# Kernel tuning notes

Hardware: AMD Instinct MI355X
Metric: run time of the kernel (lower is better)

Reference implementation:

```python
import jax, jax.numpy as jnp
import numpy as np

WS = 8          # window size
NUM_HEADS = 8


def setup_inputs() -> dict:
    key = jax.random.key(0)
    k1, k2, k3 = jax.random.split(key, 3)
    B, H, W, C = 8, 192, 192, 256
    x = jax.random.normal(k1, (B, H, W, C), dtype=jnp.float32)
    w_qkv = jax.random.normal(k2, (3 * C, C), dtype=jnp.float32) * (C ** -0.5)
    b_qkv = jnp.zeros((3 * C,), dtype=jnp.float32)
    w_proj = jax.random.normal(k3, (C, C), dtype=jnp.float32) * (C ** -0.5)
    b_proj = jnp.zeros((C,), dtype=jnp.float32)
    return {"x": x, "w_qkv": w_qkv, "b_qkv": b_qkv, "w_proj": w_proj, "b_proj": b_proj}


def _mhsa(tokens, w_qkv, b_qkv, w_proj, b_proj):
    # tokens: [Bgrp, N, C]
    Bg, N, C = tokens.shape
    d = C // NUM_HEADS
    qkv = tokens @ w_qkv.T + b_qkv                      # [Bg, N, 3C]
    qkv = qkv.reshape(Bg, N, 3, NUM_HEADS, d)
    q, k, v = [jnp.transpose(qkv[:, :, i], (0, 2, 1, 3)) for i in range(3)]  # [Bg, h, N, d]
    attn = jax.nn.softmax(jnp.einsum('bhnd,bhmd->bhnm', q, k) * (d ** -0.5), axis=-1)
    out = jnp.einsum('bhnm,bhmd->bhnd', attn, v)        # [Bg, h, N, d]
    out = jnp.transpose(out, (0, 2, 1, 3)).reshape(Bg, N, C)
    return out @ w_proj.T + b_proj


def reference(x, w_qkv, b_qkv, w_proj, b_proj):
    B, H, W, C = x.shape
    nH, nW = H // WS, W // WS
    # window partition: [B, H, W, C] -> [B*nH*nW, WS, WS, C]
    g = x.reshape(B, nH, WS, nW, WS, C).transpose(0, 1, 3, 2, 4, 5)
    tokens = g.reshape(B * nH * nW, WS * WS, C)
    tokens = _mhsa(tokens, w_qkv, b_qkv, w_proj, b_proj)
    # window unpartition
    g = tokens.reshape(B, nH, nW, WS, WS, C).transpose(0, 1, 3, 2, 4, 5)
    return g.reshape(B, H, W, C)
```

## Files before the change

### kernel.cpp

```cpp
#include <hip/hip_runtime.h>

typedef _Float16 half8  __attribute__((ext_vector_type(8)));
typedef _Float16 half4_t __attribute__((ext_vector_type(4)));
typedef __fp16   fp16x2 __attribute__((ext_vector_type(2)));
typedef float    f32x4  __attribute__((ext_vector_type(4)));

union PKU  { fp16x2 h; int i; };
union PK2  { fp16x2 h[2]; int i[2]; half4_t h4; };

__device__ __forceinline__ half4_t mk4(int a, int b) {
  PK2 u; u.i[0] = a; u.i[1] = b; return u.h4;
}

__device__ __forceinline__ int tokIdx(int r, int c) { return r*256 + (c ^ ((r & 7) << 3)); }

__global__ void __launch_bounds__(256)
wconv_kernel(const float* __restrict__ wq, const float* __restrict__ wp,
             _Float16* __restrict__ o)
{
  const int i = (blockIdx.x * 256 + threadIdx.x) * 8;
  const float4 a = *(const float4*)((i < 768*256 ? wq + i : wp + (i - 768*256)));
  const float4 b = *(const float4*)((i < 768*256 ? wq + i + 4 : wp + (i - 768*256) + 4));
  half8 h;
  h[0] = (_Float16)a.x; h[1] = (_Float16)a.y; h[2] = (_Float16)a.z; h[3] = (_Float16)a.w;
  h[4] = (_Float16)b.x; h[5] = (_Float16)b.y; h[6] = (_Float16)b.z; h[7] = (_Float16)b.w;
  *(half8*)(o + i) = h;
}

__global__ void __launch_bounds__(256, 3)
attn_kernel(const float* __restrict__ x,
            const float* __restrict__ b_qkv,
            const float* __restrict__ b_proj,
            const _Float16* __restrict__ w16,
            float* __restrict__ out)
{
  __shared__ __align__(16) _Float16 tok[64*256];

  const int tid  = threadIdx.x;
  const int lane = tid & 63;
  const int w    = tid >> 6;
  const int l15  = lane & 15;
  const int g    = lane >> 4;

  const int wid = blockIdx.x;
  const int b   = wid / (24*24);
  const int wh  = (wid / 24) % 24;
  const int ww  = wid % 24;
  const long long base = (((long long)b*192 + wh*8)*192 + ww*8)*256;

#pragma unroll
  for (int i = 0; i < 16; ++i) {
    const int tk = w*16 + i;
    const f32x4 v = *(const f32x4*)(x + base + ((tk >> 3)*192 + (tk & 7))*256 + lane*4);
    half4_t h;
    h[0] = (_Float16)v[0]; h[1] = (_Float16)v[1];
    h[2] = (_Float16)v[2]; h[3] = (_Float16)v[3];
    *(half4_t*)(tok + tk*256 + ((lane*4) ^ ((tk & 7) << 3))) = h;
  }
  __syncthreads();

  const _Float16* wqkv16  = w16;
  const _Float16* wproj16 = w16 + 768*256;

  const float ALPHA = 0.17677669529663687f;

  int ohp[2][2][4][2];

#pragma unroll
  for (int hi = 0; hi < 2; ++hi) {
    const int hd = 2*w + hi;

    int qtp[2][4][2], kcp[2][4][2];
    {
      f32x4 qa[2][4], kc[2][4];
#pragma unroll
      for (int mi = 0; mi < 2; ++mi) {
        const f32x4 bqv = *(const f32x4*)(b_qkv + hd*32 + mi*16 + g*4);
        const f32x4 bkv = *(const f32x4*)(b_qkv + 256 + hd*32 + mi*16 + g*4);
#pragma unroll
        for (int ni = 0; ni < 4; ++ni) { qa[mi][ni] = bqv; kc[mi][ni] = bkv; }
      }
#pragma unroll
      for (int kk = 0; kk < 8; ++kk) {
        half8 bt[4], awq[2], awk[2];
#pragma unroll
        for (int ni = 0; ni < 4; ++ni)
          bt[ni] = *(const half8*)(tok + tokIdx(ni*16 + l15, kk*32 + g*8));
#pragma unroll
        for (int mi = 0; mi < 2; ++mi) {
          awq[mi] = *(const half8*)(wqkv16 + (      hd*32 + mi*16 + l15)*256 + kk*32 + g*8);
          awk[mi] = *(const half8*)(wqkv16 + (256 + hd*32 + mi*16 + l15)*256 + kk*32 + g*8);
        }
        __builtin_amdgcn_s_setprio(1);
#pragma unroll
        for (int mi = 0; mi < 2; ++mi)
#pragma unroll
          for (int ni = 0; ni < 4; ++ni) {
            qa[mi][ni] = __builtin_amdgcn_mfma_f32_16x16x32_f16(awq[mi], bt[ni], qa[mi][ni], 0, 0, 0);
            kc[mi][ni] = __builtin_amdgcn_mfma_f32_16x16x32_f16(awk[mi], bt[ni], kc[mi][ni], 0, 0, 0);
          }
        __builtin_amdgcn_s_setprio(0);
      }
#pragma unroll
      for (int mi = 0; mi < 2; ++mi)
#pragma unroll
        for (int ni = 0; ni < 4; ++ni) {
          PKU q0, q1, k0, k1;
          q0.h = __builtin_amdgcn_cvt_pkrtz(qa[mi][ni][0]*ALPHA, qa[mi][ni][1]*ALPHA);
          q1.h = __builtin_amdgcn_cvt_pkrtz(qa[mi][ni][2]*ALPHA, qa[mi][ni][3]*ALPHA);
          k0.h = __builtin_amdgcn_cvt_pkrtz(kc[mi][ni][0], kc[mi][ni][1]);
          k1.h = __builtin_amdgcn_cvt_pkrtz(kc[mi][ni][2], kc[mi][ni][3]);
          qtp[mi][ni][0] = q0.i; qtp[mi][ni][1] = q1.i;
          kcp[mi][ni][0] = k0.i; kcp[mi][ni][1] = k1.i;
        }
    }

    int pk[4][4][2];
    float rv[4];
#pragma unroll
    for (int pr = 0; pr < 2; ++pr) {
      f32x4 s[4][2];
#pragma unroll
      for (int MI = 0; MI < 4; ++MI)
#pragma unroll
        for (int nj = 0; nj < 2; ++nj) s[MI][nj] = (f32x4)0.0f;
      __builtin_amdgcn_s_setprio(1);
#pragma unroll
      for (int kk2 = 0; kk2 < 2; ++kk2)
#pragma unroll
        for (int nj = 0; nj < 2; ++nj) {
          const int ni = pr*2 + nj;
          const half4_t qb = mk4(qtp[kk2][ni][0], qtp[kk2][ni][1]);
#pragma unroll
          for (int MI = 0; MI < 4; ++MI)
            s[MI][nj] = __builtin_amdgcn_mfma_f32_16x16x16f16(
                mk4(kcp[kk2][MI][0], kcp[kk2][MI][1]), qb, s[MI][nj], 0, 0, 0);
        }
      __builtin_amdgcn_s_setprio(0);

#pragma unroll
      for (int nj = 0; nj < 2; ++nj) {
        const int ni = pr*2 + nj;
        float mm[4];
#pragma unroll
        for (int MI = 0; MI < 4; ++MI)
          mm[MI] = fmaxf(fmaxf(s[MI][nj][0], s[MI][nj][1]), fmaxf(s[MI][nj][2], s[MI][nj][3]));
        float m = fmaxf(fmaxf(mm[0], mm[1]), fmaxf(mm[2], mm[3]));
        m = fmaxf(m, __shfl_xor(m, 16, 64));
        m = fmaxf(m, __shfl_xor(m, 32, 64));
        float ss[4];
#pragma unroll
        for (int MI = 0; MI < 4; ++MI) {
#pragma unroll
          for (int r = 0; r < 4; ++r) s[MI][nj][r] = __expf(s[MI][nj][r] - m);
          ss[MI] = (s[MI][nj][0] + s[MI][nj][1]) + (s[MI][nj][2] + s[MI][nj][3]);
        }
        float sum = (ss[0] + ss[1]) + (ss[2] + ss[3]);
        sum += __shfl_xor(sum, 16, 64);
        sum += __shfl_xor(sum, 32, 64);
        rv[ni] = 1.0f / sum;
#pragma unroll
        for (int MI = 0; MI < 4; ++MI) {
          PKU u0, u1;
          u0.h = __builtin_amdgcn_cvt_pkrtz(s[MI][nj][0], s[MI][nj][1]);
          u1.h = __builtin_amdgcn_cvt_pkrtz(s[MI][nj][2], s[MI][nj][3]);
          pk[MI][ni][0] = u0.i;
          pk[MI][ni][1] = u1.i;
        }
      }
    }

    int vpk[4][2][2];
    {
      f32x4 vv[4][2];
#pragma unroll
      for (int ni = 0; ni < 2; ++ni) {
        const float bv = b_qkv[512 + hd*32 + ni*16 + l15];
#pragma unroll
        for (int mi = 0; mi < 4; ++mi) vv[mi][ni] = (f32x4)bv;
      }
#pragma unroll
      for (int kk = 0; kk < 8; ++kk) {
        half8 bt[4], wv[2];
#pragma unroll
        for (int mi = 0; mi < 4; ++mi)
          bt[mi] = *(const half8*)(tok + tokIdx(mi*16 + l15, kk*32 + g*8));
#pragma unroll
        for (int ni = 0; ni < 2; ++ni)
          wv[ni] = *(const half8*)(wqkv16 + (512 + hd*32 + ni*16 + l15)*256 + kk*32 + g*8);
        __builtin_amdgcn_s_setprio(1);
#pragma unroll
        for (int mi = 0; mi < 4; ++mi)
#pragma unroll
          for (int ni = 0; ni < 2; ++ni)
            vv[mi][ni] = __builtin_amdgcn_mfma_f32_16x16x32_f16(bt[mi], wv[ni], vv[mi][ni], 0, 0, 0);
        __builtin_amdgcn_s_setprio(0);
      }
#pragma unroll
      for (int ni = 0; ni < 2; ++ni)
#pragma unroll
        for (int mi = 0; mi < 4; ++mi) {
          PKU u0, u1;
          u0.h = __builtin_amdgcn_cvt_pkrtz(vv[mi][ni][0], vv[mi][ni][1]);
          u1.h = __builtin_amdgcn_cvt_pkrtz(vv[mi][ni][2], vv[mi][ni][3]);
          vpk[mi][ni][0] = u0.i;
          vpk[mi][ni][1] = u1.i;
        }
    }

    {
      f32x4 oh[2][4];
#pragma unroll
      for (int MI = 0; MI < 2; ++MI)
#pragma unroll
        for (int ni = 0; ni < 4; ++ni) oh[MI][ni] = (f32x4)0.0f;
      __builtin_amdgcn_s_setprio(1);
#pragma unroll
      for (int kk2 = 0; kk2 < 4; ++kk2)
#pragma unroll
        for (int ni = 0; ni < 4; ++ni) {
          const half4_t pb = mk4(pk[kk2][ni][0], pk[kk2][ni][1]);
#pragma unroll
          for (int MI = 0; MI < 2; ++MI)
            oh[MI][ni] = __builtin_amdgcn_mfma_f32_16x16x16f16(
                mk4(vpk[kk2][MI][0], vpk[kk2][MI][1]), pb, oh[MI][ni], 0, 0, 0);
        }
      __builtin_amdgcn_s_setprio(0);
#pragma unroll
      for (int MI = 0; MI < 2; ++MI)
#pragma unroll
        for (int ni = 0; ni < 4; ++ni) {
          PK2 u;
          u.h[0] = __builtin_amdgcn_cvt_pkrtz(oh[MI][ni][0] * rv[ni], oh[MI][ni][1] * rv[ni]);
          u.h[1] = __builtin_amdgcn_cvt_pkrtz(oh[MI][ni][2] * rv[ni], oh[MI][ni][3] * rv[ni]);
          ohp[hi][MI][ni][0] = u.i[0];
          ohp[hi][MI][ni][1] = u.i[1];
        }
    }
  }

  __syncthreads();

#pragma unroll
  for (int hi = 0; hi < 2; ++hi) {
    const int hd = 2*w + hi;
#pragma unroll
    for (int MI = 0; MI < 2; ++MI)
#pragma unroll
      for (int ni = 0; ni < 4; ++ni) {
        PK2 u;
        u.i[0] = ohp[hi][MI][ni][0];
        u.i[1] = ohp[hi][MI][ni][1];
        *(half4_t*)(tok + tokIdx(ni*16 + l15, hd*32 + MI*16 + g*4)) = u.h4;
      }
  }
  __syncthreads();

  f32x4 pa[4][4];
#pragma unroll
  for (int ni = 0; ni < 4; ++ni) {
    const float bb = b_proj[w*64 + ni*16 + l15];
#pragma unroll
    for (int mi = 0; mi < 4; ++mi) pa[mi][ni] = (f32x4)bb;
  }

#pragma unroll
  for (int kk = 0; kk < 8; ++kk) {
    half8 af[4], bf[4];
#pragma unroll
    for (int mi = 0; mi < 4; ++mi)
      af[mi] = *(const half8*)(tok + tokIdx(mi*16 + l15, kk*32 + g*8));
#pragma unroll
    for (int ni = 0; ni < 4; ++ni)
      bf[ni] = *(const half8*)(wproj16 + (w*64 + ni*16 + l15)*256 + kk*32 + g*8);
    __builtin_amdgcn_s_setprio(1);
#pragma unroll
    for (int mi = 0; mi < 4; ++mi)
#pragma unroll
      for (int ni = 0; ni < 4; ++ni)
        pa[mi][ni] = __builtin_amdgcn_mfma_f32_16x16x32_f16(af[mi], bf[ni], pa[mi][ni], 0, 0, 0);
    __builtin_amdgcn_s_setprio(0);
  }

  float* tokF = (float*)tok;
#pragma unroll
  for (int p = 0; p < 2; ++p) {
    __syncthreads();
#pragma unroll
    for (int mh = 0; mh < 2; ++mh) {
      const int mi = 2*p + mh;
#pragma unroll
      for (int ni = 0; ni < 4; ++ni)
#pragma unroll
        for (int r = 0; r < 4; ++r) {
          const int tr = mh*16 + g*4 + r;
          tokF[tr*256 + ((w*64 + ni*16 + l15) ^ ((tr & 7) << 2))] = pa[mi][ni][r];
        }
    }
    __syncthreads();
#pragma unroll
    for (int i = 0; i < 8; ++i) {
      const int tr = w*8 + i;
      const int t  = p*32 + tr;
      const long long rowbase = base + ((long long)(t >> 3)*192 + (t & 7))*256;
      const f32x4 v4 = *(const f32x4*)(tokF + tr*256 + ((lane*4) ^ ((tr & 7) << 2)));
      *(f32x4*)(out + rowbase + lane*4) = v4;
    }
  }
}

extern "C" void kernel_launch(void* const* d_in, const int* in_sizes, int n_in,
                              void* d_out, int out_size, void* d_ws, size_t ws_size,
                              hipStream_t stream) {
  const float* x      = (const float*)d_in[0];
  const float* w_qkv  = (const float*)d_in[1];
  const float* b_qkv  = (const float*)d_in[2];
  const float* w_proj = (const float*)d_in[3];
  const float* b_proj = (const float*)d_in[4];
  float* out = (float*)d_out;
  _Float16* w16 = (_Float16*)d_ws;

  wconv_kernel<<<128, 256, 0, stream>>>(w_qkv, w_proj, w16);
  attn_kernel<<<4608, 256, 0, stream>>>(x, b_qkv, b_proj, w16, out);
}
```

Before: 337.1 us.

## Interleave V projection MFMAs with softmax of scores to overlap compute

Computes all four score tiles up front, then interleaves the V-projection MFMA steps with the per-column softmax (exp, reductions, shuffles), so that matrix-core work and VALU/transcendental work can overlap within a wave. The setprio hints around the V MFMAs are dropped. Holding all 16 score accumulators live alongside the V accumulators raises register pressure, which could cause spills or lower occupancy under the 3-blocks launch bound.

```diff
diff --git a/kernel.cpp b/kernel.cpp
--- a/kernel.cpp
+++ b/kernel.cpp
@@ -27,6 +27,54 @@
   *(half8*)(o + i) = h;
 }
 
+#define SOFTMAX_NI(ni)                                                          \
+  {                                                                             \
+    float mm0 = fmaxf(fmaxf(s[0][ni][0], s[0][ni][1]), fmaxf(s[0][ni][2], s[0][ni][3])); \
+    float mm1 = fmaxf(fmaxf(s[1][ni][0], s[1][ni][1]), fmaxf(s[1][ni][2], s[1][ni][3])); \
+    float mm2 = fmaxf(fmaxf(s[2][ni][0], s[2][ni][1]), fmaxf(s[2][ni][2], s[2][ni][3])); \
+    float mm3 = fmaxf(fmaxf(s[3][ni][0], s[3][ni][1]), fmaxf(s[3][ni][2], s[3][ni][3])); \
+    float m = fmaxf(fmaxf(mm0, mm1), fmaxf(mm2, mm3));                          \
+    m = fmaxf(m, __shfl_xor(m, 16, 64));                                        \
+    m = fmaxf(m, __shfl_xor(m, 32, 64));                                        \
+    float ss[4];                                                                \
+    _Pragma("unroll")                                                           \
+    for (int MI = 0; MI < 4; ++MI) {                                            \
+      _Pragma("unroll")                                                         \
+      for (int r = 0; r < 4; ++r) s[MI][ni][r] = __expf(s[MI][ni][r] - m);      \
+      ss[MI] = (s[MI][ni][0] + s[MI][ni][1]) + (s[MI][ni][2] + s[MI][ni][3]);   \
+    }                                                                           \
+    float sum = (ss[0] + ss[1]) + (ss[2] + ss[3]);                              \
+    sum += __shfl_xor(sum, 16, 64);                                             \
+    sum += __shfl_xor(sum, 32, 64);                                             \
+    rv[ni] = 1.0f / sum;                                                        \
+    _Pragma("unroll")                                                           \
+    for (int MI = 0; MI < 4; ++MI) {                                            \
+      PKU u0, u1;                                                               \
+      u0.h = __builtin_amdgcn_cvt_pkrtz(s[MI][ni][0], s[MI][ni][1]);            \
+      u1.h = __builtin_amdgcn_cvt_pkrtz(s[MI][ni][2], s[MI][ni][3]);            \
+      pk[MI][ni][0] = u0.i;                                                     \
+      pk[MI][ni][1] = u1.i;                                                     \
+    }                                                                           \
+  }
+
+#define V_STEP(kk)                                                              \
+  {                                                                             \
+    half8 bt0 = *(const half8*)(tok + tokIdx( 0 + l15, (kk)*32 + g*8));         \
+    half8 bt1 = *(const half8*)(tok + tokIdx(16 + l15, (kk)*32 + g*8));         \
+    half8 bt2 = *(const half8*)(tok + tokIdx(32 + l15, (kk)*32 + g*8));         \
+    half8 bt3 = *(const half8*)(tok + tokIdx(48 + l15, (kk)*32 + g*8));         \
+    half8 wv0 = *(const half8*)(wqkv16 + (512 + hd*32 +      l15)*256 + (kk)*32 + g*8); \
+    half8 wv1 = *(const half8*)(wqkv16 + (512 + hd*32 + 16 + l15)*256 + (kk)*32 + g*8); \
+    vv[0][0] = __builtin_amdgcn_mfma_f32_16x16x32_f16(bt0, wv0, vv[0][0], 0, 0, 0); \
+    vv[0][1] = __builtin_amdgcn_mfma_f32_16x16x32_f16(bt0, wv1, vv[0][1], 0, 0, 0); \
+    vv[1][0] = __builtin_amdgcn_mfma_f32_16x16x32_f16(bt1, wv0, vv[1][0], 0, 0, 0); \
+    vv[1][1] = __builtin_amdgcn_mfma_f32_16x16x32_f16(bt1, wv1, vv[1][1], 0, 0, 0); \
+    vv[2][0] = __builtin_amdgcn_mfma_f32_16x16x32_f16(bt2, wv0, vv[2][0], 0, 0, 0); \
+    vv[2][1] = __builtin_amdgcn_mfma_f32_16x16x32_f16(bt2, wv1, vv[2][1], 0, 0, 0); \
+    vv[3][0] = __builtin_amdgcn_mfma_f32_16x16x32_f16(bt3, wv0, vv[3][0], 0, 0, 0); \
+    vv[3][1] = __builtin_amdgcn_mfma_f32_16x16x32_f16(bt3, wv1, vv[3][1], 0, 0, 0); \
+  }
+
 __global__ void __launch_bounds__(256, 3)
 attn_kernel(const float* __restrict__ x,
             const float* __restrict__ b_qkv,
@@ -117,96 +165,57 @@
 
     int pk[4][4][2];
     float rv[4];
-#pragma unroll
-    for (int pr = 0; pr < 2; ++pr) {
-      f32x4 s[4][2];
+    f32x4 vv[4][2];
+    {
+      f32x4 s[4][4];
 #pragma unroll
       for (int MI = 0; MI < 4; ++MI)
 #pragma unroll
-        for (int nj = 0; nj < 2; ++nj) s[MI][nj] = (f32x4)0.0f;
+        for (int ni = 0; ni < 4; ++ni) s[MI][ni] = (f32x4)0.0f;
       __builtin_amdgcn_s_setprio(1);
 #pragma unroll
       for (int kk2 = 0; kk2 < 2; ++kk2)
 #pragma unroll
-        for (int nj = 0; nj < 2; ++nj) {
-          const int ni = pr*2 + nj;
+        for (int ni = 0; ni < 4; ++ni) {
           const half4_t qb = mk4(qtp[kk2][ni][0], qtp[kk2][ni][1]);
 #pragma unroll
           for (int MI = 0; MI < 4; ++MI)
-            s[MI][nj] = __builtin_amdgcn_mfma_f32_16x16x16f16(
-                mk4(kcp[kk2][MI][0], kcp[kk2][MI][1]), qb, s[MI][nj], 0, 0, 0);
+            s[MI][ni] = __builtin_amdgcn_mfma_f32_16x16x16f16(
+                mk4(kcp[kk2][MI][0], kcp[kk2][MI][1]), qb, s[MI][ni], 0, 0, 0);
         }
       __builtin_amdgcn_s_setprio(0);
 
-#pragma unroll
-      for (int nj = 0; nj < 2; ++nj) {
-        const int ni = pr*2 + nj;
-        float mm[4];
-#pragma unroll
-        for (int MI = 0; MI < 4; ++MI)
-          mm[MI] = fmaxf(fmaxf(s[MI][nj][0], s[MI][nj][1]), fmaxf(s[MI][nj][2], s[MI][nj][3]));
-        float m = fmaxf(fmaxf(mm[0], mm[1]), fmaxf(mm[2], mm[3]));
-        m = fmaxf(m, __shfl_xor(m, 16, 64));
-        m = fmaxf(m, __shfl_xor(m, 32, 64));
-        float ss[4];
-#pragma unroll
-        for (int MI = 0; MI < 4; ++MI) {
-#pragma unroll
-          for (int r = 0; r < 4; ++r) s[MI][nj][r] = __expf(s[MI][nj][r] - m);
-          ss[MI] = (s[MI][nj][0] + s[MI][nj][1]) + (s[MI][nj][2] + s[MI][nj][3]);
-        }
-        float sum = (ss[0] + ss[1]) + (ss[2] + ss[3]);
-        sum += __shfl_xor(sum, 16, 64);
-        sum += __shfl_xor(sum, 32, 64);
-        rv[ni] = 1.0f / sum;
-#pragma unroll
-        for (int MI = 0; MI < 4; ++MI) {
-          PKU u0, u1;
-          u0.h = __builtin_amdgcn_cvt_pkrtz(s[MI][nj][0], s[MI][nj][1]);
-          u1.h = __builtin_amdgcn_cvt_pkrtz(s[MI][nj][2], s[MI][nj][3]);
-          pk[MI][ni][0] = u0.i;
-          pk[MI][ni][1] = u1.i;
-        }
-      }
-    }
-
-    int vpk[4][2][2];
-    {
-      f32x4 vv[4][2];
 #pragma unroll
       for (int ni = 0; ni < 2; ++ni) {
         const float bv = b_qkv[512 + hd*32 + ni*16 + l15];
 #pragma unroll
         for (int mi = 0; mi < 4; ++mi) vv[mi][ni] = (f32x4)bv;
       }
-#pragma unroll
-      for (int kk = 0; kk < 8; ++kk) {
-        half8 bt[4], wv[2];
-#pragma unroll
-        for (int mi = 0; mi < 4; ++mi)
-          bt[mi] = *(const half8*)(tok + tokIdx(mi*16 + l15, kk*32 + g*8));
-#pragma unroll
-        for (int ni = 0; ni < 2; ++ni)
-          wv[ni] = *(const half8*)(wqkv16 + (512 + hd*32 + ni*16 + l15)*256 + kk*32 + g*8);
-        __builtin_amdgcn_s_setprio(1);
-#pragma unroll
-        for (int mi = 0; mi < 4; ++mi)
-#pragma unroll
-          for (int ni = 0; ni < 2; ++ni)
-            vv[mi][ni] = __builtin_amdgcn_mfma_f32_16x16x32_f16(bt[mi], wv[ni], vv[mi][ni], 0, 0, 0);
-        __builtin_amdgcn_s_setprio(0);
-      }
-#pragma unroll
-      for (int ni = 0; ni < 2; ++ni)
-#pragma unroll
-        for (int mi = 0; mi < 4; ++mi) {
-          PKU u0, u1;
-          u0.h = __builtin_amdgcn_cvt_pkrtz(vv[mi][ni][0], vv[mi][ni][1]);
-          u1.h = __builtin_amdgcn_cvt_pkrtz(vv[mi][ni][2], vv[mi][ni][3]);
-          vpk[mi][ni][0] = u0.i;
-          vpk[mi][ni][1] = u1.i;
-        }
-    }
+      V_STEP(0)
+      V_STEP(1)
+      SOFTMAX_NI(0)
+      V_STEP(2)
+      V_STEP(3)
+      SOFTMAX_NI(1)
+      V_STEP(4)
+      V_STEP(5)
+      SOFTMAX_NI(2)
+      V_STEP(6)
+      V_STEP(7)
+      SOFTMAX_NI(3)
+    }
+
+    int vpk[4][2][2];
+#pragma unroll
+    for (int ni = 0; ni < 2; ++ni)
+#pragma unroll
+      for (int mi = 0; mi < 4; ++mi) {
+        PKU u0, u1;
+        u0.h = __builtin_amdgcn_cvt_pkrtz(vv[mi][ni][0], vv[mi][ni][1]);
+        u1.h = __builtin_amdgcn_cvt_pkrtz(vv[mi][ni][2], vv[mi][ni][3]);
+        vpk[mi][ni][0] = u0.i;
+        vpk[mi][ni][1] = u1.i;
+      }
 
     {
       f32x4 oh[2][4];
```

After: 352.2 us. 4.5% more time.

## Assign one head per wave with 512-thread blocks for higher occupancy

Applied to the files above, without the earlier changes.

Doubles the block to 8 waves so each wave handles a single attention head instead of two. The Q and K projections are computed in separate phases, and the output projection splits 32 columns per wave. This cuts per-wave register pressure and raises resident waves per CU, which should hide MFMA and LDS latency better. The tighter launch bounds risk register spilling, and the larger blocks add more barrier participants.

```diff
diff --git a/kernel.cpp b/kernel.cpp
--- a/kernel.cpp
+++ b/kernel.cpp
@@ -27,7 +27,7 @@
   *(half8*)(o + i) = h;
 }
 
-__global__ void __launch_bounds__(256, 3)
+__global__ void __launch_bounds__(512, 4)
 attn_kernel(const float* __restrict__ x,
             const float* __restrict__ b_qkv,
             const float* __restrict__ b_proj,
@@ -49,8 +49,8 @@
   const long long base = (((long long)b*192 + wh*8)*192 + ww*8)*256;
 
 #pragma unroll
-  for (int i = 0; i < 16; ++i) {
-    const int tk = w*16 + i;
+  for (int i = 0; i < 8; ++i) {
+    const int tk = w*8 + i;
     const f32x4 v = *(const f32x4*)(x + base + ((tk >> 3)*192 + (tk & 7))*256 + lane*4);
     half4_t h;
     h[0] = (_Float16)v[0]; h[1] = (_Float16)v[1];
@@ -63,221 +63,241 @@
   const _Float16* wproj16 = w16 + 768*256;
 
   const float ALPHA = 0.17677669529663687f;
-
-  int ohp[2][2][4][2];
-
-#pragma unroll
-  for (int hi = 0; hi < 2; ++hi) {
-    const int hd = 2*w + hi;
-
-    int qtp[2][4][2], kcp[2][4][2];
-    {
-      f32x4 qa[2][4], kc[2][4];
-#pragma unroll
-      for (int mi = 0; mi < 2; ++mi) {
-        const f32x4 bqv = *(const f32x4*)(b_qkv + hd*32 + mi*16 + g*4);
-        const f32x4 bkv = *(const f32x4*)(b_qkv + 256 + hd*32 + mi*16 + g*4);
-#pragma unroll
-        for (int ni = 0; ni < 4; ++ni) { qa[mi][ni] = bqv; kc[mi][ni] = bkv; }
-      }
-#pragma unroll
-      for (int kk = 0; kk < 8; ++kk) {
-        half8 bt[4], awq[2], awk[2];
+  const int hd = w;
+
+  int qtp[2][4][2];
+  {
+    f32x4 qa[2][4];
+#pragma unroll
+    for (int mi = 0; mi < 2; ++mi) {
+      const f32x4 bqv = *(const f32x4*)(b_qkv + hd*32 + mi*16 + g*4);
+#pragma unroll
+      for (int ni = 0; ni < 4; ++ni) qa[mi][ni] = bqv;
+    }
+#pragma unroll
+    for (int kk = 0; kk < 8; ++kk) {
+      half8 bt[4], aw[2];
+#pragma unroll
+      for (int ni = 0; ni < 4; ++ni)
+        bt[ni] = *(const half8*)(tok + tokIdx(ni*16 + l15, kk*32 + g*8));
+#pragma unroll
+      for (int mi = 0; mi < 2; ++mi)
+        aw[mi] = *(const half8*)(wqkv16 + (hd*32 + mi*16 + l15)*256 + kk*32 + g*8);
+      __builtin_amdgcn_s_setprio(1);
+#pragma unroll
+      for (int mi = 0; mi < 2; ++mi)
 #pragma unroll
         for (int ni = 0; ni < 4; ++ni)
-          bt[ni] = *(const half8*)(tok + tokIdx(ni*16 + l15, kk*32 + g*8));
-#pragma unroll
-        for (int mi = 0; mi < 2; ++mi) {
-          awq[mi] = *(const half8*)(wqkv16 + (      hd*32 + mi*16 + l15)*256 + kk*32 + g*8);
-          awk[mi] = *(const half8*)(wqkv16 + (256 + hd*32 + mi*16 + l15)*256 + kk*32 + g*8);
-        }
-        __builtin_amdgcn_s_setprio(1);
-#pragma unroll
-        for (int mi = 0; mi < 2; ++mi)
-#pragma unroll
-          for (int ni = 0; ni < 4; ++ni) {
-            qa[mi][ni] = __builtin_amdgcn_mfma_f32_16x16x32_f16(awq[mi], bt[ni], qa[mi][ni], 0, 0, 0);
-            kc[mi][ni] = __builtin_amdgcn_mfma_f32_16x16x32_f16(awk[mi], bt[ni], kc[mi][ni], 0, 0, 0);
-          }
-        __builtin_amdgcn_s_setprio(0);
-      }
+          qa[mi][ni] = __builtin_amdgcn_mfma_f32_16x16x32_f16(aw[mi], bt[ni], qa[mi][ni], 0, 0, 0);
+      __builtin_amdgcn_s_setprio(0);
+    }
+#pragma unroll
+    for (int mi = 0; mi < 2; ++mi)
+#pragma unroll
+      for (int ni = 0; ni < 4; ++ni) {
+        PKU u0, u1;
+        u0.h = __builtin_amdgcn_cvt_pkrtz(qa[mi][ni][0]*ALPHA, qa[mi][ni][1]*ALPHA);
+        u1.h = __builtin_amdgcn_cvt_pkrtz(qa[mi][ni][2]*ALPHA, qa[mi][ni][3]*ALPHA);
+        qtp[mi][ni][0] = u0.i; qtp[mi][ni][1] = u1.i;
+      }
+  }
+
+  int kcp[2][4][2];
+  {
+    f32x4 kc[2][4];
+#pragma unroll
+    for (int mi = 0; mi < 2; ++mi) {
+      const f32x4 bkv = *(const f32x4*)(b_qkv + 256 + hd*32 + mi*16 + g*4);
+#pragma unroll
+      for (int ni = 0; ni < 4; ++ni) kc[mi][ni] = bkv;
+    }
+#pragma unroll
+    for (int kk = 0; kk < 8; ++kk) {
+      half8 bt[4], aw[2];
+#pragma unroll
+      for (int ni = 0; ni < 4; ++ni)
+        bt[ni] = *(const half8*)(tok + tokIdx(ni*16 + l15, kk*32 + g*8));
 #pragma unroll
       for (int mi = 0; mi < 2; ++mi)
-#pragma unroll
-        for (int ni = 0; ni < 4; ++ni) {
-          PKU q0, q1, k0, k1;
-          q0.h = __builtin_amdgcn_cvt_pkrtz(qa[mi][ni][0]*ALPHA, qa[mi][ni][1]*ALPHA);
-          q1.h = __builtin_amdgcn_cvt_pkrtz(qa[mi][ni][2]*ALPHA, qa[mi][ni][3]*ALPHA);
-          k0.h = __builtin_amdgcn_cvt_pkrtz(kc[mi][ni][0], kc[mi][ni][1]);
-          k1.h = __builtin_amdgcn_cvt_pkrtz(kc[mi][ni][2], kc[mi][ni][3]);
-          qtp[mi][ni][0] = q0.i; qtp[mi][ni][1] = q1.i;
-          kcp[mi][ni][0] = k0.i; kcp[mi][ni][1] = k1.i;
-        }
-    }
-
-    int pk[4][4][2];
-    float rv[4];
-#pragma unroll
-    for (int pr = 0; pr < 2; ++pr) {
-      f32x4 s[4][2];
-#pragma unroll
-      for (int MI = 0; MI < 4; ++MI)
-#pragma unroll
-        for (int nj = 0; nj < 2; ++nj) s[MI][nj] = (f32x4)0.0f;
+        aw[mi] = *(const half8*)(wqkv16 + (256 + hd*32 + mi*16 + l15)*256 + kk*32 + g*8);
       __builtin_amdgcn_s_setprio(1);
 #pragma unroll
-      for (int kk2 = 0; kk2 < 2; ++kk2)
-#pragma unroll
-        for (int nj = 0; nj < 2; ++nj) {
-          const int ni = pr*2 + nj;
-          const half4_t qb = mk4(qtp[kk2][ni][0], qtp[kk2][ni][1]);
-#pragma unroll
-          for (int MI = 0; MI < 4; ++MI)
-            s[MI][nj] = __builtin_amdgcn_mfma_f32_16x16x16f16(
-                mk4(kcp[kk2][MI][0], kcp[kk2][MI][1]), qb, s[MI][nj], 0, 0, 0);
-        }
+      for (int mi = 0; mi < 2; ++mi)
+#pragma unroll
+        for (int ni = 0; ni < 4; ++ni)
+          kc[mi][ni] = __builtin_amdgcn_mfma_f32_16x16x32_f16(aw[mi], bt[ni], kc[mi][ni], 0, 0, 0);
       __builtin_amdgcn_s_setprio(0);
-
+    }
+#pragma unroll
+    for (int mi = 0; mi < 2; ++mi)
+#pragma unroll
+      for (int ni = 0; ni < 4; ++ni) {
+        PKU u0, u1;
+        u0.h = __builtin_amdgcn_cvt_pkrtz(kc[mi][ni][0], kc[mi][ni][1]);
+        u1.h = __builtin_amdgcn_cvt_pkrtz(kc[mi][ni][2], kc[mi][ni][3]);
+        kcp[mi][ni][0] = u0.i; kcp[mi][ni][1] = u1.i;
+      }
+  }
+
+  int pk[4][4][2];
+  float rv[4];
+#pragma unroll
+  for (int pr = 0; pr < 2; ++pr) {
+    f32x4 s[4][2];
+#pragma unroll
+    for (int MI = 0; MI < 4; ++MI)
+#pragma unroll
+      for (int nj = 0; nj < 2; ++nj) s[MI][nj] = (f32x4)0.0f;
+    __builtin_amdgcn_s_setprio(1);
+#pragma unroll
+    for (int kk2 = 0; kk2 < 2; ++kk2)
 #pragma unroll
       for (int nj = 0; nj < 2; ++nj) {
         const int ni = pr*2 + nj;
-        float mm[4];
+        const half4_t qb = mk4(qtp[kk2][ni][0], qtp[kk2][ni][1]);
 #pragma unroll
         for (int MI = 0; MI < 4; ++MI)
-          mm[MI] = fmaxf(fmaxf(s[MI][nj][0], s[MI][nj][1]), fmaxf(s[MI][nj][2], s[MI][nj][3]));
-        float m = fmaxf(fmaxf(mm[0], mm[1]), fmaxf(mm[2], mm[3]));
-        m = fmaxf(m, __shfl_xor(m, 16, 64));
-        m = fmaxf(m, __shfl_xor(m, 32, 64));
-        float ss[4];
-#pragma unroll
-        for (int MI = 0; MI < 4; ++MI) {
-#pragma unroll
-          for (int r = 0; r < 4; ++r) s[MI][nj][r] = __expf(s[MI][nj][r] - m);
-          ss[MI] = (s[MI][nj][0] + s[MI][nj][1]) + (s[MI][nj][2] + s[MI][nj][3]);
-        }
-        float sum = (ss[0] + ss[1]) + (ss[2] + ss[3]);
-        sum += __shfl_xor(sum, 16, 64);
-        sum += __shfl_xor(sum, 32, 64);
-        rv[ni] = 1.0f / sum;
-#pragma unroll
-        for (int MI = 0; MI < 4; ++MI) {
-          PKU u0, u1;
-          u0.h = __builtin_amdgcn_cvt_pkrtz(s[MI][nj][0], s[MI][nj][1]);
-          u1.h = __builtin_amdgcn_cvt_pkrtz(s[MI][nj][2], s[MI][nj][3]);
-          pk[MI][ni][0] = u0.i;
-          pk[MI][ni][1] = u1.i;
-        }
-      }
-    }
-
-    int vpk[4][2][2];
-    {
-      f32x4 vv[4][2];
-#pragma unroll
-      for (int ni = 0; ni < 2; ++ni) {
-        const float bv = b_qkv[512 + hd*32 + ni*16 + l15];
-#pragma unroll
-        for (int mi = 0; mi < 4; ++mi) vv[mi][ni] = (f32x4)bv;
-      }
-#pragma unroll
-      for (int kk = 0; kk < 8; ++kk) {
-        half8 bt[4], wv[2];
-#pragma unroll
-        for (int mi = 0; mi < 4; ++mi)
-          bt[mi] = *(const half8*)(tok + tokIdx(mi*16 + l15, kk*32 + g*8));
+          s[MI][nj] = __builtin_amdgcn_mfma_f32_16x16x16f16(
+              mk4(kcp[kk2][MI][0], kcp[kk2][MI][1]), qb, s[MI][nj], 0, 0, 0);
+      }
+    __builtin_amdgcn_s_setprio(0);
+
+#pragma unroll
+    for (int nj = 0; nj < 2; ++nj) {
+      const int ni = pr*2 + nj;
+      float mm[4];
+#pragma unroll
+      for (int MI = 0; MI < 4; ++MI)
+        mm[MI] = fmaxf(fmaxf(s[MI][nj][0], s[MI][nj][1]), fmaxf(s[MI][nj][2], s[MI][nj][3]));
+      float m = fmaxf(fmaxf(mm[0], mm[1]), fmaxf(mm[2], mm[3]));
+      m = fmaxf(m, __shfl_xor(m, 16, 64));
+      m = fmaxf(m, __shfl_xor(m, 32, 64));
+      float ss[4];
+#pragma unroll
+      for (int MI = 0; MI < 4; ++MI) {
+#pragma unroll
+        for (int r = 0; r < 4; ++r) s[MI][nj][r] = __expf(s[MI][nj][r] - m);
+        ss[MI] = (s[MI][nj][0] + s[MI][nj][1]) + (s[MI][nj][2] + s[MI][nj][3]);
+      }
+      float sum = (ss[0] + ss[1]) + (ss[2] + ss[3]);
+      sum += __shfl_xor(sum, 16, 64);
+      sum += __shfl_xor(sum, 32, 64);
+      rv[ni] = 1.0f / sum;
+#pragma unroll
+      for (int MI = 0; MI < 4; ++MI) {
+        PKU u0, u1;
+        u0.h = __builtin_amdgcn_cvt_pkrtz(s[MI][nj][0], s[MI][nj][1]);
+        u1.h = __builtin_amdgcn_cvt_pkrtz(s[MI][nj][2], s[MI][nj][3]);
+        pk[MI][ni][0] = u0.i;
+        pk[MI][ni][1] = u1.i;
+      }
+    }
+  }
+
+  int vpk[4][2][2];
+  {
+    f32x4 vv[4][2];
+#pragma unroll
+    for (int ni = 0; ni < 2; ++ni) {
+      const float bv = b_qkv[512 + hd*32 + ni*16 + l15];
+#pragma unroll
+      for (int mi = 0; mi < 4; ++mi) vv[mi][ni] = (f32x4)bv;
+    }
+#pragma unroll
+    for (int kk = 0; kk < 8; ++kk) {
+      half8 bt[4], wv[2];
+#pragma unroll
+      for (int mi = 0; mi < 4; ++mi)
+        bt[mi] = *(const half8*)(tok + tokIdx(mi*16 + l15, kk*32 + g*8));
+#pragma unroll
+      for (int ni = 0; ni < 2; ++ni)
+        wv[ni] = *(const half8*)(wqkv16 + (512 + hd*32 + ni*16 + l15)*256 + kk*32 + g*8);
+      __builtin_amdgcn_s_setprio(1);
+#pragma unroll
+      for (int mi = 0; mi < 4; ++mi)
 #pragma unroll
         for (int ni = 0; ni < 2; ++ni)
-          wv[ni] = *(const half8*)(wqkv16 + (512 + hd*32 + ni*16 + l15)*256 + kk*32 + g*8);
-        __builtin_amdgcn_s_setprio(1);
-#pragma unroll
-        for (int mi = 0; mi < 4; ++mi)
-#pragma unroll
-          for (int ni = 0; ni < 2; ++ni)
-            vv[mi][ni] = __builtin_amdgcn_mfma_f32_16x16x32_f16(bt[mi], wv[ni], vv[mi][ni], 0, 0, 0);
-        __builtin_amdgcn_s_setprio(0);
-      }
-#pragma unroll
-      for (int ni = 0; ni < 2; ++ni)
-#pragma unroll
-        for (int mi = 0; mi < 4; ++mi) {
-          PKU u0, u1;
-          u0.h = __builtin_amdgcn_cvt_pkrtz(vv[mi][ni][0], vv[mi][ni][1]);
-          u1.h = __builtin_amdgcn_cvt_pkrtz(vv[mi][ni][2], vv[mi][ni][3]);
-          vpk[mi][ni][0] = u0.i;
-          vpk[mi][ni][1] = u1.i;
-        }
-    }
-
-    {
-      f32x4 oh[2][4];
-#pragma unroll
-      for (int MI = 0; MI < 2; ++MI)
-#pragma unroll
-        for (int ni = 0; ni < 4; ++ni) oh[MI][ni] = (f32x4)0.0f;
-      __builtin_amdgcn_s_setprio(1);
-#pragma unroll
-      for (int kk2 = 0; kk2 < 4; ++kk2)
-#pragma unroll
-        for (int ni = 0; ni < 4; ++ni) {
-          const half4_t pb = mk4(pk[kk2][ni][0], pk[kk2][ni][1]);
-#pragma unroll
-          for (int MI = 0; MI < 2; ++MI)
-            oh[MI][ni] = __builtin_amdgcn_mfma_f32_16x16x16f16(
-                mk4(vpk[kk2][MI][0], vpk[kk2][MI][1]), pb, oh[MI][ni], 0, 0, 0);
-        }
+          vv[mi][ni] = __builtin_amdgcn_mfma_f32_16x16x32_f16(bt[mi], wv[ni], vv[mi][ni], 0, 0, 0);
       __builtin_amdgcn_s_setprio(0);
-#pragma unroll
-      for (int MI = 0; MI < 2; ++MI)
-#pragma unroll
-        for (int ni = 0; ni < 4; ++ni) {
-          PK2 u;
-          u.h[0] = __builtin_amdgcn_cvt_pkrtz(oh[MI][ni][0] * rv[ni], oh[MI][ni][1] * rv[ni]);
-          u.h[1] = __builtin_amdgcn_cvt_pkrtz(oh[MI][ni][2] * rv[ni], oh[MI][ni][3] * rv[ni]);
-          ohp[hi][MI][ni][0] = u.i[0];
-          ohp[hi][MI][ni][1] = u.i[1];
-        }
-    }
-  }
-
-  __syncthreads();
-
-#pragma unroll
-  for (int hi = 0; hi < 2; ++hi) {
-    const int hd = 2*w + hi;
+    }
+#pragma unroll
+    for (int ni = 0; ni < 2; ++ni)
+#pragma unroll
+      for (int mi = 0; mi < 4; ++mi) {
+        PKU u0, u1;
+        u0.h = __builtin_amdgcn_cvt_pkrtz(vv[mi][ni][0], vv[mi][ni][1]);
+        u1.h = __builtin_amdgcn_cvt_pkrtz(vv[mi][ni][2], vv[mi][ni][3]);
+        vpk[mi][ni][0] = u0.i;
+        vpk[mi][ni][1] = u1.i;
+      }
+  }
+
+  int ohp[2][4][2];
+  {
+    f32x4 oh[2][4];
+#pragma unroll
+    for (int MI = 0; MI < 2; ++MI)
+#pragma unroll
+      for (int ni = 0; ni < 4; ++ni) oh[MI][ni] = (f32x4)0.0f;
+    __builtin_amdgcn_s_setprio(1);
+#pragma unroll
+    for (int kk2 = 0; kk2 < 4; ++kk2)
+#pragma unroll
+      for (int ni = 0; ni < 4; ++ni) {
+        const half4_t pb = mk4(pk[kk2][ni][0], pk[kk2][ni][1]);
+#pragma unroll
+        for (int MI = 0; MI < 2; ++MI)
+          oh[MI][ni] = __builtin_amdgcn_mfma_f32_16x16x16f16(
+              mk4(vpk[kk2][MI][0], vpk[kk2][MI][1]), pb, oh[MI][ni], 0, 0, 0);
+      }
+    __builtin_amdgcn_s_setprio(0);
 #pragma unroll
     for (int MI = 0; MI < 2; ++MI)
 #pragma unroll
       for (int ni = 0; ni < 4; ++ni) {
         PK2 u;
-        u.i[0] = ohp[hi][MI][ni][0];
-        u.i[1] = ohp[hi][MI][ni][1];
-        *(half4_t*)(tok + tokIdx(ni*16 + l15, hd*32 + MI*16 + g*4)) = u.h4;
-      }
-  }
+        u.h[0] = __builtin_amdgcn_cvt_pkrtz(oh[MI][ni][0] * rv[ni], oh[MI][ni][1] * rv[ni]);
+        u.h[1] = __builtin_amdgcn_cvt_pkrtz(oh[MI][ni][2] * rv[ni], oh[MI][ni][3] * rv[ni]);
+        ohp[MI][ni][0] = u.i[0];
+        ohp[MI][ni][1] = u.i[1];
+      }
+  }
+
   __syncthreads();
 
-  f32x4 pa[4][4];
-#pragma unroll
-  for (int ni = 0; ni < 4; ++ni) {
-    const float bb = b_proj[w*64 + ni*16 + l15];
+#pragma unroll
+  for (int MI = 0; MI < 2; ++MI)
+#pragma unroll
+    for (int ni = 0; ni < 4; ++ni) {
+      PK2 u;
+      u.i[0] = ohp[MI][ni][0];
+      u.i[1] = ohp[MI][ni][1];
+      *(half4_t*)(tok + tokIdx(ni*16 + l15, hd*32 + MI*16 + g*4)) = u.h4;
+    }
+  __syncthreads();
+
+  f32x4 pa[4][2];
+#pragma unroll
+  for (int ni = 0; ni < 2; ++ni) {
+    const float bb = b_proj[w*32 + ni*16 + l15];
 #pragma unroll
     for (int mi = 0; mi < 4; ++mi) pa[mi][ni] = (f32x4)bb;
   }
 
 #pragma unroll
   for (int kk = 0; kk < 8; ++kk) {
-    half8 af[4], bf[4];
+    half8 af[4], bf[2];
 #pragma unroll
     for (int mi = 0; mi < 4; ++mi)
       af[mi] = *(const half8*)(tok + tokIdx(mi*16 + l15, kk*32 + g*8));
 #pragma unroll
-    for (int ni = 0; ni < 4; ++ni)
-      bf[ni] = *(const half8*)(wproj16 + (w*64 + ni*16 + l15)*256 + kk*32 + g*8);
+    for (int ni = 0; ni < 2; ++ni)
+      bf[ni] = *(const half8*)(wproj16 + (w*32 + ni*16 + l15)*256 + kk*32 + g*8);
     __builtin_amdgcn_s_setprio(1);
 #pragma unroll
     for (int mi = 0; mi < 4; ++mi)
 #pragma unroll
-      for (int ni = 0; ni < 4; ++ni)
+      for (int ni = 0; ni < 2; ++ni)
         pa[mi][ni] = __builtin_amdgcn_mfma_f32_16x16x32_f16(af[mi], bf[ni], pa[mi][ni], 0, 0, 0);
     __builtin_amdgcn_s_setprio(0);
   }
@@ -290,17 +310,17 @@
     for (int mh = 0; mh < 2; ++mh) {
       const int mi = 2*p + mh;
 #pragma unroll
-      for (int ni = 0; ni < 4; ++ni)
+      for (int ni = 0; ni < 2; ++ni)
 #pragma unroll
         for (int r = 0; r < 4; ++r) {
           const int tr = mh*16 + g*4 + r;
-          tokF[tr*256 + ((w*64 + ni*16 + l15) ^ ((tr & 7) << 2))] = pa[mi][ni][r];
+          tokF[tr*256 + ((w*32 + ni*16 + l15) ^ ((tr & 7) << 2))] = pa[mi][ni][r];
         }
     }
     __syncthreads();
 #pragma unroll
-    for (int i = 0; i < 8; ++i) {
-      const int tr = w*8 + i;
+    for (int i = 0; i < 4; ++i) {
+      const int tr = w*4 + i;
       const int t  = p*32 + tr;
       const long long rowbase = base + ((long long)(t >> 3)*192 + (t & 7))*256;
       const f32x4 v4 = *(const f32x4*)(tokF + tr*256 + ((lane*4) ^ ((tr & 7) << 2)));
@@ -321,5 +341,5 @@
   _Float16* w16 = (_Float16*)d_ws;
 
   wconv_kernel<<<128, 256, 0, stream>>>(w_qkv, w_proj, w16);
-  attn_kernel<<<4608, 256, 0, stream>>>(x, b_qkv, b_proj, w16, out);
+  attn_kernel<<<4608, 512, 0, stream>>>(x, b_qkv, b_proj, w16, out);
 }
```

Result: slower. 356.8 us (+5.8%).
